# Performance work log

Hardware: AMD Instinct MI355X
Metric: run time of the kernel (lower is better)

## Reference

```python
import jax, jax.numpy as jnp
import numpy as np
import math

B, T, D = 2, 2048, 1024
H, HD = 16, 64
MAX_LEN = 2048


def _build_rope_sin_cos(max_seq, head_dim):
    inv_freq = 1.0 / 10000 ** (jnp.arange(0, head_dim, 2) / head_dim)
    positions = jnp.arange(max_seq)
    sinusoid_inp = jnp.einsum('i,j->ij', positions.astype(jnp.float32), inv_freq.astype(jnp.float32))
    sin = jnp.repeat(jnp.sin(sinusoid_inp), 2, axis=-1)
    cos = jnp.repeat(jnp.cos(sinusoid_inp), 2, axis=-1)
    return sin, cos


def _rotate_half(x):
    x1 = x[..., ::2]
    x2 = x[..., 1::2]
    return jnp.stack((-x2, x1), axis=-1).reshape(x.shape)


def setup_inputs() -> dict:
    key = jax.random.key(0)
    ks = jax.random.split(key, 6)
    x = jax.random.normal(ks[0], (B, T, D), dtype=jnp.float32)
    # causal boolean mask (B, T, T)
    mask = jnp.broadcast_to(jnp.tril(jnp.ones((T, T), dtype=bool)), (B, T, T))
    s = 1.0 / math.sqrt(D)
    wq = jax.random.normal(ks[1], (D, H, HD), dtype=jnp.float32) * s
    wk = jax.random.normal(ks[2], (D, H, HD), dtype=jnp.float32) * s
    wv = jax.random.normal(ks[3], (D, H, HD), dtype=jnp.float32) * s
    wo = jax.random.normal(ks[4], (H * HD, D), dtype=jnp.float32) * (1.0 / math.sqrt(H * HD))
    return {"x": x, "mask": mask, "wq": wq, "wk": wk, "wv": wv, "wo": wo}


def reference(x, mask, wq, wk, wv, wo):
    Bx, Tx, Dx = x.shape
    # q/k/v projections: DenseGeneral D -> (H, HD)
    q = jnp.einsum('btd,dhe->bthe', x, wq)
    k = jnp.einsum('btd,dhe->bthe', x, wk)
    v = jnp.einsum('btd,dhe->bthe', x, wv)
    sin, cos = _build_rope_sin_cos(MAX_LEN, HD)
    sin_t = sin[:Tx][None, :, None, :]
    cos_t = cos[:Tx][None, :, None, :]
    q = q * cos_t + _rotate_half(q) * sin_t
    k = k * cos_t + _rotate_half(k) * sin_t
    q = jnp.transpose(q, (0, 2, 1, 3))  # (B,H,T,HD)
    k = jnp.transpose(k, (0, 2, 1, 3))
    v = jnp.transpose(v, (0, 2, 1, 3))
    scale = 1.0 / math.sqrt(HD)
    logits = jnp.einsum('bhqd,bhkd->bhqk', q, k) * scale
    mask_f = mask[:, None, :, :].astype(jnp.float32)
    logits = logits + (1.0 - mask_f) * -1e10
    w = jax.nn.softmax(logits, axis=-1)
    attn_out = jnp.einsum('bhqk,bhkd->bhqd', w, v)
    attn_out = jnp.transpose(attn_out, (0, 2, 1, 3)).reshape(Bx, Tx, -1)
    return attn_out @ wo
```

## Files before the change

### kernel.cpp

```cpp
#include <hip/hip_runtime.h>
#include <cstdint>
#include <cstddef>

typedef __bf16 bf16x8 __attribute__((ext_vector_type(8)));
typedef __bf16 bf16x2 __attribute__((ext_vector_type(2)));
typedef float f32x4 __attribute__((ext_vector_type(4)));
typedef float f32x16 __attribute__((ext_vector_type(16)));
typedef unsigned int u32x4 __attribute__((ext_vector_type(4)));
#define UNROLL _Pragma("unroll")

__device__ __forceinline__ unsigned short f2bf(float f) {
  unsigned int x = __builtin_bit_cast(unsigned int, f);
  x += 0x7fffu + ((x >> 16) & 1u);
  return (unsigned short)(x >> 16);
}
__device__ __forceinline__ float bf2f(unsigned short u) {
  return __builtin_bit_cast(float, (unsigned int)u << 16);
}
__device__ __forceinline__ unsigned int cvtpk(float a, float b) {
  bf16x2 t; t[0] = (__bf16)a; t[1] = (__bf16)b;
  return __builtin_bit_cast(unsigned int, t);
}
__device__ __forceinline__ void async16(const void* g, void* l) {
  __builtin_amdgcn_global_load_lds((void __attribute__((address_space(1)))*)g,
                                   (void __attribute__((address_space(3)))*)l,
                                   16, 0, 0);
}

__global__ void prep_x(const float* __restrict__ x, unsigned short* __restrict__ xb) {
  int i = blockIdx.x * 256 + threadIdx.x;
  const float4* p = (const float4*)(x + (size_t)i * 8);
  float4 a = p[0], b = p[1];
  ushort4 o0 = {f2bf(a.x), f2bf(a.y), f2bf(a.z), f2bf(a.w)};
  ushort4 o1 = {f2bf(b.x), f2bf(b.y), f2bf(b.z), f2bf(b.w)};
  ushort4* q = (ushort4*)(xb + (size_t)i * 8);
  q[0] = o0; q[1] = o1;
}

__global__ void prep_w(const float* __restrict__ wq, const float* __restrict__ wk,
                       const float* __restrict__ wv, const float* __restrict__ wo,
                       unsigned short* __restrict__ out) {
  __shared__ float tile[32][33];
  const float* src = blockIdx.z == 0 ? wq : blockIdx.z == 1 ? wk : blockIdx.z == 2 ? wv : wo;
  unsigned short* dst = out + (size_t)blockIdx.z * 1048576;
  int kb = blockIdx.x * 32, nb = blockIdx.y * 32;
  int c = threadIdx.x & 31, r4 = (threadIdx.x >> 5) * 4;
UNROLL
  for (int i = 0; i < 4; ++i)
    tile[r4 + i][c] = src[(size_t)(kb + r4 + i) * 1024 + nb + c];
  __syncthreads();
UNROLL
  for (int i = 0; i < 4; ++i)
    dst[(size_t)(nb + r4 + i) * 1024 + kb + c] = f2bf(tile[c][r4 + i]);
}

__global__ void prep_rope(float2* __restrict__ tab) {
  int idx = blockIdx.x * 256 + threadIdx.x;
  int t = idx >> 5, i = idx & 31;
  float inv = exp2f(-(float)i * (13.287712379549449f / 32.0f));
  float ang = (float)t * inv;
  tab[idx] = make_float2(cosf(ang), sinf(ang));
}

__global__ __launch_bounds__(256, 3) void gemmqkv(
    const unsigned short* __restrict__ A, const unsigned short* __restrict__ Bt,
    unsigned short* __restrict__ qout, unsigned short* __restrict__ kout,
    unsigned short* __restrict__ vtout, const float2* __restrict__ rope) {
  __shared__ __align__(16) unsigned short As[128 * 64];
  __shared__ __align__(16) unsigned short Bs[128 * 64];
  const int tid = threadIdx.x;
  const int lane = tid & 63, wid = tid >> 6;
  const int wr = wid >> 1, wc = wid & 1;
  const int g = lane >> 4, r16 = lane & 15;
  const int m0 = blockIdx.y * 128, n0 = blockIdx.x * 128;

  f32x4 acc[4][4];
UNROLL
  for (int i = 0; i < 4; ++i)
UNROLL
    for (int j = 0; j < 4; ++j) acc[i][j] = (f32x4){0.f, 0.f, 0.f, 0.f};

  const int ce = (((tid & 7) ^ ((tid >> 3) & 7)) << 3);
  const unsigned short* gA = A + (size_t)(m0 + (tid >> 3)) * 1024 + ce;
  const unsigned short* gB = Bt + (size_t)(n0 + (tid >> 3)) * 1024 + ce;
  char* lA = (char*)As + tid * 16;
  char* lB = (char*)Bs + tid * 16;

  const int swz = (r16 & 7) << 4;

  for (int u = 0; u < 16; ++u) {
    const int k0 = u * 64;
UNROLL
    for (int s = 0; s < 4; ++s) {
      async16(gA + (size_t)s * 32 * 1024 + k0, lA + s * 4096);
      async16(gB + (size_t)s * 32 * 1024 + k0, lB + s * 4096);
    }
    __syncthreads();
UNROLL
    for (int kk = 0; kk < 2; ++kk) {
      bf16x8 af[4], bfr[4];
UNROLL
      for (int mi = 0; mi < 4; ++mi)
        af[mi] = *(const bf16x8*)((const char*)As +
                  (wr * 64 + mi * 16 + r16) * 128 + ((kk * 64 + g * 16) ^ swz));
UNROLL
      for (int ni = 0; ni < 4; ++ni)
        bfr[ni] = *(const bf16x8*)((const char*)Bs +
                  (wc * 64 + ni * 16 + r16) * 128 + ((kk * 64 + g * 16) ^ swz));
UNROLL
      for (int mi = 0; mi < 4; ++mi)
UNROLL
        for (int ni = 0; ni < 4; ++ni)
          acc[mi][ni] = __builtin_amdgcn_mfma_f32_16x16x32_bf16(af[mi], bfr[ni],
                                                                acc[mi][ni], 0, 0, 0);
    }
    __syncthreads();
  }

  const int which = n0 >> 10;
  const int b = (m0 >= 2048) ? 1 : 0;
  const float QSCL = 0.18033688011112042f;
UNROLL
  for (int mi = 0; mi < 4; ++mi) {
    const int rowb = m0 + wr * 64 + mi * 16 + g * 4;
    const int trow = rowb & 2047;
UNROLL
    for (int ni = 0; ni < 4; ++ni) {
      const int n = n0 + wc * 64 + ni * 16 + r16;
      const int h = (n >> 6) & 15, e = n & 63;
      f32x4 v = acc[mi][ni];
      if (which < 2) {
        const int fi = e >> 1;
        const bool ev = (e & 1) == 0;
UNROLL
        for (int j = 0; j < 4; ++j) {
          float2 cs = rope[(trow + j) * 32 + fi];
          float p = __shfl_xor(v[j], 1);
          v[j] = ev ? (v[j] * cs.x - p * cs.y) : (v[j] * cs.x + p * cs.y);
        }
        if (which == 0) { v[0] *= QSCL; v[1] *= QSCL; v[2] *= QSCL; v[3] *= QSCL; }
      }
      if (which == 2) {
        size_t base = (((size_t)b * 16 + h) * 64 + e) * 2048 + trow;
        ushort4 pkv = {f2bf(v[0]), f2bf(v[1]), f2bf(v[2]), f2bf(v[3])};
        *(ushort4*)(vtout + base) = pkv;
      } else {
        unsigned short* dst = (which == 0) ? qout : kout;
        size_t base = (((size_t)b * 16 + h) * 2048 + trow) * 64 + e;
UNROLL
        for (int j = 0; j < 4; ++j) dst[base + (size_t)j * 64] = f2bf(v[j]);
      }
    }
  }
}

__global__ __launch_bounds__(256, 4) void gemm_o(
    const unsigned short* __restrict__ A, const unsigned short* __restrict__ Bt,
    float* __restrict__ out) {
  __shared__ __align__(16) unsigned short As[64 * 64];
  __shared__ __align__(16) unsigned short Bs[64 * 64];
  const int tid = threadIdx.x;
  const int lane = tid & 63, wid = tid >> 6;
  const int wm = wid >> 1, wn = wid & 1;
  const int g = lane >> 4, r16 = lane & 15;
  const int m0 = blockIdx.y * 64, n0 = blockIdx.x * 64;

  f32x4 acc[2][2];
UNROLL
  for (int i = 0; i < 2; ++i)
UNROLL
    for (int j = 0; j < 2; ++j) acc[i][j] = (f32x4){0.f, 0.f, 0.f, 0.f};

  const int ce = (((tid & 7) ^ ((tid >> 3) & 7)) << 3);
  const unsigned short* gA = A + (size_t)(m0 + (tid >> 3)) * 1024 + ce;
  const unsigned short* gB = Bt + (size_t)(n0 + (tid >> 3)) * 1024 + ce;
  char* lA = (char*)As + tid * 16;
  char* lB = (char*)Bs + tid * 16;
  const int swz = (r16 & 7) << 4;

  for (int u = 0; u < 16; ++u) {
    const int k0 = u * 64;
UNROLL
    for (int s = 0; s < 2; ++s) {
      async16(gA + (size_t)s * 32 * 1024 + k0, lA + s * 4096);
      async16(gB + (size_t)s * 32 * 1024 + k0, lB + s * 4096);
    }
    __syncthreads();
UNROLL
    for (int kk = 0; kk < 2; ++kk) {
      bf16x8 af[2], bfr[2];
UNROLL
      for (int mi = 0; mi < 2; ++mi)
        af[mi] = *(const bf16x8*)((const char*)As +
                  (wm * 32 + mi * 16 + r16) * 128 + ((kk * 64 + g * 16) ^ swz));
UNROLL
      for (int ni = 0; ni < 2; ++ni)
        bfr[ni] = *(const bf16x8*)((const char*)Bs +
                  (wn * 32 + ni * 16 + r16) * 128 + ((kk * 64 + g * 16) ^ swz));
UNROLL
      for (int mi = 0; mi < 2; ++mi)
UNROLL
        for (int ni = 0; ni < 2; ++ni)
          acc[mi][ni] = __builtin_amdgcn_mfma_f32_16x16x32_bf16(af[mi], bfr[ni],
                                                                acc[mi][ni], 0, 0, 0);
    }
    __syncthreads();
  }

UNROLL
  for (int mi = 0; mi < 2; ++mi) {
    const int rowb = m0 + wm * 32 + mi * 16 + g * 4;
UNROLL
    for (int ni = 0; ni < 2; ++ni) {
      const int n = n0 + wn * 32 + ni * 16 + r16;
UNROLL
      for (int j = 0; j < 4; ++j)
        out[(size_t)(rowb + j) * 1024 + n] = acc[mi][ni][j];
    }
  }
}

__device__ const signed char c_qt[32]   = {15,15,10,10,15,14,14,14,13, 9, 9, 4,13,13,12,12, 8, 8,12,11,11,11, 7, 7, 3, 6, 6, 5, 5, 2, 1, 0};
__device__ const signed char c_t0[32]   = { 0,11, 0,11,22, 0,10,20, 0, 0,10, 0,10,19, 0, 9, 0, 9,18, 0, 8,16, 0, 8, 0, 0, 7, 0, 6, 0, 0, 0};
__device__ const signed char c_len[32]  = {11,11,11,11,10,10,10,10,10,10,10,10, 9, 9, 9, 9, 9, 9, 8, 8, 8, 8, 8, 8, 8, 7, 7, 6, 6, 6, 4, 2};
__device__ const signed char c_slot[32] = {24,25,10,11,26,21,22,23,18, 8, 9,-1,19,20,15,16, 6, 7,17,12,13,14, 4, 5,-1, 2, 3, 0, 1,-1,-1,-1};

__global__ __launch_bounds__(256, 3) void attn4(
    const unsigned short* __restrict__ qb, const unsigned short* __restrict__ kb,
    const unsigned short* __restrict__ vtb, unsigned short* __restrict__ attnb,
    unsigned short* __restrict__ po, float* __restrict__ ml) {
  __shared__ __align__(16) char smem[2][16384];
  const int tid = threadIdx.x;
  const int lane = tid & 63, w = tid >> 6;
  const int l31 = lane & 31, h = lane >> 5;
  const int bh = blockIdx.x;
  const int item = blockIdx.y;
  const int qt = c_qt[item];
  const int t0 = c_t0[item];
  const int t1 = t0 + c_len[item];
  const int slot = c_slot[item];
  const int q0w = qt * 128 + w * 32;
  const int qg = q0w + l31;
  const size_t kvbase = (size_t)bh * (2048 * 64);
  const float FM = 11.0f;

  bf16x8 qf[4];
  const unsigned short* qp = qb + kvbase + (size_t)qg * 64 + h * 8;
UNROLL
  for (int kk = 0; kk < 4; ++kk) qf[kk] = *(const bf16x8*)(qp + kk * 16);

  const int lr = lane >> 3;
  const int cb2 = ((lane & 7) ^ lr) << 3;
  const bool isK = (w < 2);
  const int c0 = isK ? w * 4 : (w - 2) * 4;
  const unsigned short* srcp[4];
  int dstoff[4];
  const size_t step = isK ? 4096 : 64;
UNROLL
  for (int s = 0; s < 4; ++s) {
    int r = (c0 + s) * 8 + lr;
    srcp[s] = isK ? (kb + kvbase + (size_t)r * 64 + cb2)
                  : (vtb + kvbase + (size_t)r * 2048 + cb2);
    dstoff[s] = (w * 4 + s) * 1024 + lane * 16;
  }

  f32x16 o0, o1;
UNROLL
  for (int r = 0; r < 16; ++r) { o0[r] = 0.f; o1[r] = 0.f; }
  float l_run = 0.f;

UNROLL
  for (int s = 0; s < 4; ++s) async16(srcp[s] + (size_t)t0 * step, &smem[0][0] + dstoff[s]);
  __syncthreads();

  const int swz = (l31 & 7) << 4;
  for (int t = t0; t < t1; ++t) {
    const int kt0 = t << 6;
    if (t + 1 < t1) {
      char* db = &smem[(t + 1 - t0) & 1][0];
UNROLL
      for (int s = 0; s < 4; ++s)
        async16(srcp[s] + (size_t)(t + 1) * step, db + dstoff[s]);
    }
    if (kt0 <= q0w + 31) {
      const char* cbuf = &smem[(t - t0) & 1][0];
      f32x16 sa, sb;
UNROLL
      for (int r = 0; r < 16; ++r) { sa[r] = 0.f; sb[r] = 0.f; }
      __builtin_amdgcn_s_setprio(1);
UNROLL
      for (int kk = 0; kk < 4; ++kk) {
        bf16x8 kf = *(const bf16x8*)(cbuf + l31 * 128 + ((kk * 32 + h * 16) ^ swz));
        sa = __builtin_amdgcn_mfma_f32_32x32x16_bf16(kf, qf[kk], sa, 0, 0, 0);
      }
UNROLL
      for (int kk = 0; kk < 4; ++kk) {
        bf16x8 kf = *(const bf16x8*)(cbuf + (32 + l31) * 128 + ((kk * 32 + h * 16) ^ swz));
        sb = __builtin_amdgcn_mfma_f32_32x32x16_bf16(kf, qf[kk], sb, 0, 0, 0);
      }
      __builtin_amdgcn_s_setprio(0);
      if (kt0 + 63 > q0w) {
UNROLL
        for (int r = 0; r < 16; ++r) {
          int koff = (r & 3) + 8 * (r >> 2) + 4 * h;
          if (kt0 + koff > qg) sa[r] = -3e38f;
          if (kt0 + 32 + koff > qg) sb[r] = -3e38f;
        }
      }
UNROLL
      for (int r = 0; r < 16; ++r) {
        sa[r] = exp2f(sa[r] - FM);
        sb[r] = exp2f(sb[r] - FM);
      }
      float ts[16];
UNROLL
      for (int i = 0; i < 16; ++i) ts[i] = sa[i] + sb[i];
UNROLL
      for (int i = 0; i < 8; ++i) ts[i] += ts[i + 8];
UNROLL
      for (int i = 0; i < 4; ++i) ts[i] += ts[i + 4];
      ts[0] += ts[2]; ts[1] += ts[3];
      float ps = ts[0] + ts[1];
      ps += __shfl_xor(ps, 32);
      l_run += ps;
      unsigned int lo[8], hi[8];
UNROLL
      for (int b8 = 0; b8 < 4; ++b8) {
        lo[b8]     = cvtpk(sa[4 * b8], sa[4 * b8 + 1]);
        hi[b8]     = cvtpk(sa[4 * b8 + 2], sa[4 * b8 + 3]);
        lo[4 + b8] = cvtpk(sb[4 * b8], sb[4 * b8 + 1]);
        hi[4 + b8] = cvtpk(sb[4 * b8 + 2], sb[4 * b8 + 3]);
      }
      bf16x8 pa[4];
UNROLL
      for (int j = 0; j < 4; ++j) {
        const int bb = (j >> 1) * 4 + (j & 1) * 2;
        unsigned int a0 = lo[bb], b0 = lo[bb + 1];
        unsigned int a1 = hi[bb], b1 = hi[bb + 1];
        asm volatile("v_permlane32_swap_b32 %0, %1" : "+v"(a0), "+v"(b0));
        asm volatile("v_permlane32_swap_b32 %0, %1" : "+v"(a1), "+v"(b1));
        u32x4 f;
        f[0] = a0; f[1] = a1; f[2] = b0; f[3] = b1;
        pa[j] = __builtin_bit_cast(bf16x8, f);
      }
      __builtin_amdgcn_s_setprio(1);
UNROLL
      for (int j = 0; j < 4; ++j) {
        bf16x8 v0 = *(const bf16x8*)(cbuf + 8192 + l31 * 128 + ((j * 32 + h * 16) ^ swz));
        bf16x8 v1 = *(const bf16x8*)(cbuf + 8192 + (32 + l31) * 128 + ((j * 32 + h * 16) ^ swz));
        o0 = __builtin_amdgcn_mfma_f32_32x32x16_bf16(pa[j], v0, o0, 0, 0, 0);
        o1 = __builtin_amdgcn_mfma_f32_32x32x16_bf16(pa[j], v1, o1, 0, 0, 0);
      }
      __builtin_amdgcn_s_setprio(0);
    }
    __syncthreads();
  }

  float* lsh = (float*)&smem[0][0] + w * 32;
  if (h == 0) lsh[l31] = 1.0f / l_run;
  __syncthreads();
  f32x4 inv[4];
UNROLL
  for (int rg = 0; rg < 4; ++rg) inv[rg] = *(const f32x4*)&lsh[8 * rg + 4 * h];
  if (slot < 0) {
    const int b = bh >> 4, hh = bh & 15;
UNROLL
    for (int r = 0; r < 16; ++r) {
      const int qg2 = q0w + (r & 3) + 8 * (r >> 2) + 4 * h;
      const size_t base = (((size_t)b * 2048 + qg2) * 16 + hh) * 64 + l31;
      const float iv = inv[r >> 2][r & 3];
      attnb[base]      = f2bf(o0[r] * iv);
      attnb[base + 32] = f2bf(o1[r] * iv);
    }
  } else {
    const int p = bh * 27 + slot;
    if (h == 0) ml[p * 128 + w * 32 + l31] = l_run;
    unsigned short* pb = po + (size_t)p * 8192;
UNROLL
    for (int r = 0; r < 16; ++r) {
      const int rl = w * 32 + (r & 3) + 8 * (r >> 2) + 4 * h;
      const float iv = inv[r >> 2][r & 3];
      pb[rl * 64 + l31]      = f2bf(o0[r] * iv);
      pb[rl * 64 + l31 + 32] = f2bf(o1[r] * iv);
    }
  }
}

__global__ void attn_combine(const unsigned short* __restrict__ po,
                             const float* __restrict__ ml,
                             unsigned short* __restrict__ attnb) {
  const int idx = blockIdx.x * 256 + threadIdx.x;
  const int cg = idx & 3;
  const int row = (idx >> 2) & 127;
  const int t2 = idx >> 9;
  const int qi = t2 % 11;
  const int bh = t2 / 11;
  const int qt = qi + 5;
  const int cnt = (qt < 11) ? 2 : 3;
  const int base = (qt < 11) ? (qt - 5) * 2 : 12 + (qt - 11) * 3;
  const int slotg = bh * 27 + base;
  float acc[16];
UNROLL
  for (int i = 0; i < 16; ++i) acc[i] = 0.f;
  float wsum = 0.f;
  for (int i = 0; i < cnt; ++i) {
    const float l = ml[(slotg + i) * 128 + row];
    wsum += l;
    const ushort4* p = (const ushort4*)(po + (size_t)(slotg + i) * 8192 + row * 64 + cg * 16);
UNROLL
    for (int v = 0; v < 4; ++v) {
      ushort4 u = p[v];
      acc[v * 4 + 0] += l * bf2f(u.x);
      acc[v * 4 + 1] += l * bf2f(u.y);
      acc[v * 4 + 2] += l * bf2f(u.z);
      acc[v * 4 + 3] += l * bf2f(u.w);
    }
  }
  const float inv = 1.0f / wsum;
  const int b = bh >> 4, hh = bh & 15;
  const int q = qt * 128 + row;
  ushort4* out = (ushort4*)(attnb + (((size_t)b * 2048 + q) * 16 + hh) * 64 + cg * 16);
UNROLL
  for (int v = 0; v < 4; ++v) {
    ushort4 o;
    o.x = f2bf(acc[v * 4 + 0] * inv);
    o.y = f2bf(acc[v * 4 + 1] * inv);
    o.z = f2bf(acc[v * 4 + 2] * inv);
    o.w = f2bf(acc[v * 4 + 3] * inv);
    out[v] = o;
  }
}

extern "C" void kernel_launch(void* const* d_in, const int* in_sizes, int n_in,
                              void* d_out, int out_size, void* d_ws, size_t ws_size,
                              hipStream_t stream) {
  (void)in_sizes; (void)n_in; (void)out_size; (void)ws_size;
  const float* x = (const float*)d_in[0];
  const float* wq = (const float*)d_in[2];
  const float* wk = (const float*)d_in[3];
  const float* wv = (const float*)d_in[4];
  const float* wo = (const float*)d_in[5];

  unsigned short* xb = (unsigned short*)d_ws;
  unsigned short* wT = xb + 4 * 1024 * 1024;
  float2* rope = (float2*)(wT + 4 * 1024 * 1024);
  unsigned short* qb = (unsigned short*)(rope + 65536);
  unsigned short* kbuf = qb + 4 * 1024 * 1024;
  unsigned short* vtb = kbuf + 4 * 1024 * 1024;
  unsigned short* attnb = vtb + 4 * 1024 * 1024;

  unsigned short* po = xb;
  float* mlb = (float*)rope;

  prep_x<<<dim3(2048), dim3(256), 0, stream>>>(x, xb);
  prep_w<<<dim3(32, 32, 4), dim3(256), 0, stream>>>(wq, wk, wv, wo, wT);
  prep_rope<<<dim3(256), dim3(256), 0, stream>>>(rope);
  gemmqkv<<<dim3(24, 32), dim3(256), 0, stream>>>(xb, wT, qb, kbuf, vtb, rope);
  attn4<<<dim3(32, 32), dim3(256), 0, stream>>>(qb, kbuf, vtb, attnb, po, mlb);
  attn_combine<<<dim3(704), dim3(256), 0, stream>>>(po, mlb, attnb);
  gemm_o<<<dim3(16, 64), dim3(256), 0, stream>>>(attnb, wT + 3 * 1024 * 1024,
                                                 (float*)d_out);
}
```

Baseline: 111.8 us.

## Double-buffer output GEMM loads and use vmcnt waits in attention pipeline

The output-projection GEMM now double-buffers its A/B tiles in LDS, so the next K-slice's async loads are issued before the current slice's MFMAs, with explicit vmcnt waits and raw barriers in place of __syncthreads. The attention kernel replaces its post-prefetch __syncthreads with a partial vmcnt wait plus s_barrier, so the current tile is consumed while the next one is still in flight. The fixed-max subtraction is folded into the accumulator initial value to save a subtract per element, and attention occupancy is raised to 4 blocks per SM through launch bounds. This risks register spills at the higher occupancy, and depends on the hand-written waitcnt values matching the number of outstanding loads.

After: 111.5 us. Within noise of the previous version (-0.3%).

```diff
diff --git a/kernel.cpp b/kernel.cpp
--- a/kernel.cpp
+++ b/kernel.cpp
@@ -157,8 +157,8 @@
 __global__ __launch_bounds__(256, 4) void gemm_o(
     const unsigned short* __restrict__ A, const unsigned short* __restrict__ Bt,
     float* __restrict__ out) {
-  __shared__ __align__(16) unsigned short As[64 * 64];
-  __shared__ __align__(16) unsigned short Bs[64 * 64];
+  __shared__ __align__(16) unsigned short As[2][64 * 64];
+  __shared__ __align__(16) unsigned short Bs[2][64 * 64];
   const int tid = threadIdx.x;
   const int lane = tid & 63, wid = tid >> 6;
   const int wm = wid >> 1, wn = wid & 1;
@@ -174,28 +174,34 @@
   const int ce = (((tid & 7) ^ ((tid >> 3) & 7)) << 3);
   const unsigned short* gA = A + (size_t)(m0 + (tid >> 3)) * 1024 + ce;
   const unsigned short* gB = Bt + (size_t)(n0 + (tid >> 3)) * 1024 + ce;
-  char* lA = (char*)As + tid * 16;
-  char* lB = (char*)Bs + tid * 16;
+  const int dst0 = tid * 16;
   const int swz = (r16 & 7) << 4;
 
+#define OSTG(bb, koff) { \
+    async16(gA + (koff),             (char*)As[bb] + dst0); \
+    async16(gA + 32 * 1024 + (koff), (char*)As[bb] + dst0 + 4096); \
+    async16(gB + (koff),             (char*)Bs[bb] + dst0); \
+    async16(gB + 32 * 1024 + (koff), (char*)Bs[bb] + dst0 + 4096); }
+
+  OSTG(0, 0)
   for (int u = 0; u < 16; ++u) {
-    const int k0 = u * 64;
-UNROLL
-    for (int s = 0; s < 2; ++s) {
-      async16(gA + (size_t)s * 32 * 1024 + k0, lA + s * 4096);
-      async16(gB + (size_t)s * 32 * 1024 + k0, lB + s * 4096);
-    }
-    __syncthreads();
+    const int bsel = u & 1;
+    if (u + 1 < 16) { OSTG(bsel ^ 1, (u + 1) * 64) }
+    __builtin_amdgcn_sched_barrier(0);
+    if (u + 1 < 16) { asm volatile("s_waitcnt vmcnt(4)" ::: "memory"); }
+    else            { asm volatile("s_waitcnt vmcnt(0)" ::: "memory"); }
+    __builtin_amdgcn_s_barrier();
+    __builtin_amdgcn_sched_barrier(0);
 UNROLL
     for (int kk = 0; kk < 2; ++kk) {
       bf16x8 af[2], bfr[2];
 UNROLL
       for (int mi = 0; mi < 2; ++mi)
-        af[mi] = *(const bf16x8*)((const char*)As +
+        af[mi] = *(const bf16x8*)((const char*)As[bsel] +
                   (wm * 32 + mi * 16 + r16) * 128 + ((kk * 64 + g * 16) ^ swz));
 UNROLL
       for (int ni = 0; ni < 2; ++ni)
-        bfr[ni] = *(const bf16x8*)((const char*)Bs +
+        bfr[ni] = *(const bf16x8*)((const char*)Bs[bsel] +
                   (wn * 32 + ni * 16 + r16) * 128 + ((kk * 64 + g * 16) ^ swz));
 UNROLL
       for (int mi = 0; mi < 2; ++mi)
@@ -204,8 +210,10 @@
           acc[mi][ni] = __builtin_amdgcn_mfma_f32_16x16x32_bf16(af[mi], bfr[ni],
                                                                 acc[mi][ni], 0, 0, 0);
     }
-    __syncthreads();
-  }
+    __builtin_amdgcn_sched_barrier(0);
+    __builtin_amdgcn_s_barrier();
+  }
+#undef OSTG
 
 UNROLL
   for (int mi = 0; mi < 2; ++mi) {
@@ -225,7 +233,7 @@
 __device__ const signed char c_len[32]  = {11,11,11,11,10,10,10,10,10,10,10,10, 9, 9, 9, 9, 9, 9, 8, 8, 8, 8, 8, 8, 8, 7, 7, 6, 6, 6, 4, 2};
 __device__ const signed char c_slot[32] = {24,25,10,11,26,21,22,23,18, 8, 9,-1,19,20,15,16, 6, 7,17,12,13,14, 4, 5,-1, 2, 3, 0, 1,-1,-1,-1};
 
-__global__ __launch_bounds__(256, 3) void attn4(
+__global__ __launch_bounds__(256, 4) void attn4(
     const unsigned short* __restrict__ qb, const unsigned short* __restrict__ kb,
     const unsigned short* __restrict__ vtb, unsigned short* __restrict__ attnb,
     unsigned short* __restrict__ po, float* __restrict__ ml) {
@@ -242,7 +250,7 @@
   const int q0w = qt * 128 + w * 32;
   const int qg = q0w + l31;
   const size_t kvbase = (size_t)bh * (2048 * 64);
-  const float FM = 11.0f;
+  const float NFM = -11.0f;
 
   bf16x8 qf[4];
   const unsigned short* qp = qb + kvbase + (size_t)qg * 64 + h * 8;
@@ -271,7 +279,6 @@
 
 UNROLL
   for (int s = 0; s < 4; ++s) async16(srcp[s] + (size_t)t0 * step, &smem[0][0] + dstoff[s]);
-  __syncthreads();
 
   const int swz = (l31 & 7) << 4;
   for (int t = t0; t < t1; ++t) {
@@ -281,12 +288,19 @@
 UNROLL
       for (int s = 0; s < 4; ++s)
         async16(srcp[s] + (size_t)(t + 1) * step, db + dstoff[s]);
-    }
+      __builtin_amdgcn_sched_barrier(0);
+      asm volatile("s_waitcnt vmcnt(4)" ::: "memory");
+    } else {
+      __builtin_amdgcn_sched_barrier(0);
+      asm volatile("s_waitcnt vmcnt(0)" ::: "memory");
+    }
+    __builtin_amdgcn_s_barrier();
+    __builtin_amdgcn_sched_barrier(0);
     if (kt0 <= q0w + 31) {
       const char* cbuf = &smem[(t - t0) & 1][0];
       f32x16 sa, sb;
 UNROLL
-      for (int r = 0; r < 16; ++r) { sa[r] = 0.f; sb[r] = 0.f; }
+      for (int r = 0; r < 16; ++r) { sa[r] = NFM; sb[r] = NFM; }
       __builtin_amdgcn_s_setprio(1);
 UNROLL
       for (int kk = 0; kk < 4; ++kk) {
@@ -309,8 +323,8 @@
       }
 UNROLL
       for (int r = 0; r < 16; ++r) {
-        sa[r] = exp2f(sa[r] - FM);
-        sb[r] = exp2f(sb[r] - FM);
+        sa[r] = exp2f(sa[r]);
+        sb[r] = exp2f(sb[r]);
       }
       float ts[16];
 UNROLL
@@ -353,7 +367,8 @@
       }
       __builtin_amdgcn_s_setprio(0);
     }
-    __syncthreads();
+    __builtin_amdgcn_sched_barrier(0);
+    __builtin_amdgcn_s_barrier();
   }
 
   float* lsh = (float*)&smem[0][0] + w * 32;
```
